# Optimization experiments

Hardware: AMD Instinct MI355X
Metric: run time of the kernel (lower is better)

The kernel has to match this reference:

```python
import jax, jax.numpy as jnp
import numpy as np

BS, T, N, E = 4, 6, 400, 3000
D = 100        # object_dim == state_dim == out_fts (forced by code)
NS = 30        # num states
NOBJ = 300     # object vocab
NET = 10       # n edge types
NSTEPS = 3     # GatedGraphConv n_steps


def setup_inputs() -> dict:
    key = jax.random.key(0)
    ks = jax.random.split(key, 16)
    def nrm(k, shape, s=0.05):
        return jax.random.normal(k, shape, jnp.float32) * s
    return dict(
        class_names=jax.random.randint(ks[0], (BS, T, N), 0, NOBJ),
        states=jax.random.uniform(ks[1], (BS, T, N, NS), jnp.float32),
        edges=jax.random.randint(ks[2], (BS, T, E, 2), 0, N),
        edge_types=jax.random.randint(ks[3], (BS, T, E), 0, NET),
        visibility=jax.random.uniform(ks[4], (BS, T, N), jnp.float32),
        mask_edges=jnp.ones((BS, T, E), jnp.float32),
        obj_emb=nrm(ks[5], (NOBJ, D)),
        state_W=nrm(ks[6], (D, NS)), state_b=jnp.zeros((D,), jnp.float32),
        c1_W=nrm(ks[7], (D, 2 * D)), c1_b=jnp.zeros((D,), jnp.float32),
        c2_W=nrm(ks[8], (D, D)), c2_b=jnp.zeros((D,), jnp.float32),
        edge_embed=nrm(ks[9], (NET, D * D)),
        g_wih=nrm(ks[10], (3 * D, D)), g_whh=nrm(ks[11], (3 * D, D)),
        g_bih=jnp.zeros((3 * D,), jnp.float32), g_bhh=jnp.zeros((3 * D,), jnp.float32),
        o_wih=nrm(ks[12], (3 * D, D)), o_whh=nrm(ks[13], (3 * D, D)),
    )


def _gru(x, h, wih, whh, bih=None, bhh=None):
    # torch.nn.GRUCell semantics
    gi = x @ wih.T
    gh = h @ whh.T
    if bih is not None:
        gi = gi + bih
        gh = gh + bhh
    ir, iz, inn = jnp.split(gi, 3, axis=-1)
    hr, hz, hn = jnp.split(gh, 3, axis=-1)
    r = jax.nn.sigmoid(ir + hr)
    z = jax.nn.sigmoid(iz + hz)
    n = jnp.tanh(inn + r * hn)
    return (1.0 - z) * n + z * h


def reference(class_names, states, edges, edge_types, visibility, mask_edges,
              obj_emb, state_W, state_b, c1_W, c1_b, c2_W, c2_b,
              edge_embed, g_wih, g_whh, g_bih, g_bhh, o_wih, o_whh):
    bs, t_len, n = class_names.shape
    # initial node representation (ClassNameStateRepresentation)
    emb = obj_emb[class_names]                       # [bs,T,N,D]
    st = states @ state_W.T + state_b                # [bs,T,N,D]
    x = jnp.concatenate([emb, st], -1)
    x = jax.nn.relu(x @ c1_W.T + c1_b) @ c2_W.T + c2_b  # [bs,T,N,D]

    off = (jnp.arange(bs) * n)[:, None]              # flatten batch into node axis
    h = jnp.zeros((bs * n, D), x.dtype)              # outer temporal GRU state
    reprs = []
    for t in range(t_len):
        h = _gru(x[:, t].reshape(bs * n, D), h, o_wih, o_whh)  # bias=False
        feat_flat = h                                 # [bs*N, D]
        src = (edges[:, t, :, 0] + off).reshape(-1)   # [bs*E]
        dst = (edges[:, t, :, 1] + off).reshape(-1)
        # per-edge DxD matrices, masked (as in original)
        W = edge_embed[edge_types[:, t].reshape(-1)].reshape(-1, D, D)
        W = W * mask_edges[:, t].reshape(-1)[:, None, None]
        # NOTE: original never updates feat_flat inside the n_steps loop,
        # so every step reads the same source features; we replicate that.
        feat_out = feat_flat
        for _ in range(NSTEPS):
            msg = jnp.einsum('eij,ej->ei', W, feat_flat[src])           # per-edge matvec
            a = jax.ops.segment_sum(msg, dst, num_segments=bs * n)     # scatter-add
            feat_out = _gru(a, feat_flat, g_wih, g_whh, g_bih, g_bhh)
        reprs.append(feat_out.reshape(bs, n, D) * visibility[:, t, :, None])
    node_reprs = jnp.stack(reprs, 1)                  # [bs,T,N,D]
    num_nodes = visibility.sum(-1) + 1e-9             # [bs,T]
    global_repr = (node_reprs * visibility[..., None]).sum(2) / num_nodes[..., None]
    return node_reprs, global_repr
```

## Files before the change

### kernel.cpp

```cpp
#include <hip/hip_runtime.h>

#define BSZ   4
#define TT    6
#define NNODE 400
#define EED   3000
#define DDIM  100
#define NSDIM 30
#define NETYP 10
#define BN    (BSZ*NNODE)
#define NROW  (BSZ*TT*NNODE)
#define NEDGE (BSZ*TT*EED)
#define KPAD  1024

#define OFF_PRE1 0
#define OFF_QT   30000
#define OFF_BQ   33000
#define OFF_BF   33104
#define OFF_WIT  33408
#define OFF_BI   63408
#define OFF_BH   63744
#define OFF_WFH  64080
#define OFF_WFL  85584
#define OFF_WOH  107088
#define OFF_WOL  128592
#define OFF_BWPK 150096
#define OFF_WHPK 322128
#define OFF_HALL 343632
#define OFF_START 1303632
#define OFF_SE   1313236
#define OFF_INV  1457248
#define OFF_GI   1457280
#define OFF_UB   4682880

typedef __attribute__((ext_vector_type(8))) short bf16x8;
typedef __attribute__((ext_vector_type(4))) float f32x4;

__device__ __forceinline__ float sigf(float v) { return 1.0f / (1.0f + expf(-v)); }

__device__ __forceinline__ short bfc(float f) {
    union { float f; unsigned u; } v; v.f = f;
    unsigned r = v.u + 0x7fffu + ((v.u >> 16) & 1u);
    return (short)(r >> 16);
}

__device__ __forceinline__ float bf2f(short h) {
    union { unsigned u; float f; } x; x.u = ((unsigned)(unsigned short)h) << 16;
    return x.f;
}

__device__ __forceinline__ unsigned cvtpk(float lo, float hi) {
    unsigned r;
    asm("v_cvt_pk_bf16_f32 %0, %1, %2" : "=v"(r) : "v"(lo), "v"(hi));
    return r;
}

__global__ __launch_bounds__(256) void k_front(
    const float* __restrict__ obj_emb, const float* __restrict__ c1_W,
    const float* __restrict__ c1_b, const float* __restrict__ state_W,
    const float* __restrict__ state_b, const float* __restrict__ c2_W,
    const float* __restrict__ c2_b, const float* __restrict__ o_wih,
    const float* __restrict__ o_whh, const float* __restrict__ g_wih,
    const float* __restrict__ g_whh,
    const float* __restrict__ g_bih, const float* __restrict__ g_bhh,
    const float* __restrict__ vis, const int* __restrict__ edges,
    const int* __restrict__ etype, const float* __restrict__ emask,
    float* __restrict__ pre1, float* __restrict__ QT, float* __restrict__ bQ,
    float* __restrict__ bfold, float* __restrict__ WiT,
    float* __restrict__ bI, float* __restrict__ bH,
    ushort* __restrict__ WFH, ushort* __restrict__ WFL,
    ushort* __restrict__ WOH, ushort* __restrict__ WOL,
    ushort* __restrict__ WHpku,
    float* __restrict__ inv_nv, float* __restrict__ gout,
    int* __restrict__ start, int2* __restrict__ sortedE2) {
    int tid = threadIdx.x;
    if (blockIdx.x < 24) {
        __shared__ int hcnt[400];
        __shared__ int hstart[400];
        int c = blockIdx.x;
        int t = c >> 2, b = c & 3;
        int febase = (b * TT + t) * EED;
        for (int i = tid; i < 400; i += 256) hcnt[i] = 0;
        __syncthreads();
        for (int i = tid; i < EED; i += 256)
            atomicAdd(&hcnt[edges[(febase + i) * 2 + 1]], 1);
        __syncthreads();
        if (tid < 64) {
            int lane = tid, carry = 0;
            for (int ch = 0; ch < 7; ++ch) {
                int idx = ch * 64 + lane;
                int orig = (idx < 400) ? hcnt[idx] : 0;
                int v = orig;
                #pragma unroll
                for (int off = 1; off < 64; off <<= 1) {
                    int u = __shfl_up(v, off, 64);
                    if (lane >= off) v += u;
                }
                if (idx < 400) hstart[idx] = carry + (v - orig);
                carry += __shfl(v, 63, 64);
            }
        }
        __syncthreads();
        for (int i = tid; i < 400; i += 256) {
            start[c * 400 + i] = c * EED + hstart[i];
            hcnt[i] = hstart[i];
        }
        if (c == 23 && tid == 0) start[NROW] = NEDGE;
        __syncthreads();
        for (int i = tid; i < EED; i += 256) {
            int fe = febase + i;
            int2 ed = *(const int2*)(edges + fe * 2);
            int pos = atomicAdd(&hcnt[ed.y], 1);
            int g = etype[fe];
            float m = emask[fe];
            sortedE2[c * EED + pos] = make_int2(ed.x | (g << 16), __float_as_int(m));
        }
        return;
    }
    int i = (blockIdx.x - 24) * 256 + tid;
    if (i < 30000) {
        int cls = i / DDIM, d1 = i % DDIM;
        float acc = 0.f;
        for (int k = 0; k < DDIM; ++k)
            acc += obj_emb[cls * DDIM + k] * c1_W[d1 * 2 * DDIM + k];
        pre1[i] = acc;
    } else if (i < 33000) {
        int j = i - 30000, s = j / DDIM, d1 = j % DDIM;
        float acc = 0.f;
        for (int d = 0; d < DDIM; ++d)
            acc += c1_W[d1 * 2 * DDIM + DDIM + d] * state_W[d * NSDIM + s];
        QT[j] = acc;
    } else if (i < 33100) {
        int d1 = i - 33000;
        float acc = c1_b[d1];
        for (int d = 0; d < DDIM; ++d)
            acc += state_b[d] * c1_W[d1 * 2 * DDIM + DDIM + d];
        bQ[d1] = acc;
    } else if (i < 33400) {
        int o = i - 33100;
        float acc = 0.f;
        for (int d = 0; d < DDIM; ++d)
            acc += o_wih[o * DDIM + d] * c2_b[d];
        bfold[o] = acc;
    } else if (i < 76408) {
        int e = i - 33400;
        int j = e & 7, frag = e >> 3;
        int l = frag & 63, ct = (frag >> 6) % 21, kt = frag / (21 * 64);
        int col = ct * 16 + (l & 15);
        int gate = col / 112, dd = col % 112;
        int k = kt * 32 + ((l >> 4) << 3) + j;
        float v = 0.f;
        if (k < DDIM && dd < DDIM) {
            int o = gate * DDIM + dd;
            for (int d = 0; d < DDIM; ++d)
                v += o_wih[o * DDIM + d] * c2_W[d * DDIM + k];
        }
        short hi = bfc(v);
        WFH[frag * 8 + j] = (ushort)hi;
        WFL[frag * 8 + j] = (ushort)bfc(v - bf2f(hi));
    } else if (i < 119416) {
        int e = i - 76408;
        int j = e & 7, frag = e >> 3;
        int l = frag & 63, ct = (frag >> 6) % 21, kt = frag / (21 * 64);
        int col = ct * 16 + (l & 15);
        int gate = col / 112, dd = col % 112;
        int k = kt * 32 + ((l >> 4) << 3) + j;
        float v = 0.f;
        if (k < DDIM && dd < DDIM)
            v = o_whh[(gate * DDIM + dd) * DDIM + k];
        short hi = bfc(v);
        WOH[frag * 8 + j] = (ushort)hi;
        WOL[frag * 8 + j] = (ushort)bfc(v - bf2f(hi));
    } else if (i < 149416) {
        int j = i - 119416, k = j / 300, o = j % 300;
        WiT[j] = g_wih[o * DDIM + k];
    } else if (i < 149752) {
        int col = i - 149416, gate = col / 112, o = col % 112;
        bI[col] = (o < DDIM) ? g_bih[gate * DDIM + o] : 0.f;
    } else if (i < 150088) {
        int col = i - 149752, gate = col / 112, o = col % 112;
        bH[col] = (o < DDIM) ? g_bhh[gate * DDIM + o] : 0.f;
    } else if (i >= 150144 && i < 151680) {
        int g = (i - 150144) >> 6;
        int lane = i & 63;
        float s = 0.f;
        for (int n = lane; n < NNODE; n += 64)
            s += vis[g * NNODE + n];
        #pragma unroll
        for (int off = 32; off > 0; off >>= 1)
            s += __shfl_down(s, off, 64);
        if (lane == 0) inv_nv[g] = 1.f / (s + 1e-9f);
    } else if (i >= 151680 && i < 154080) {
        gout[i - 151680] = 0.f;
    } else if (i >= 154080 && i < 197088) {
        int e = i - 154080;
        int j = e & 7, frag = e >> 3;
        int l = frag & 63, ct = (frag >> 6) % 21, kt2 = frag / (21 * 64);
        int col = ct * 16 + (l & 15);
        int gate = col / 112, o = col % 112;
        int k = kt2 * 32 + ((l >> 4) << 3) + j;
        float v = (k < DDIM && o < DDIM)
                  ? g_whh[(gate * DDIM + o) * DDIM + k] : 0.f;
        WHpku[frag * 8 + j] = (ushort)bfc(v);
    }
}

__global__ __launch_bounds__(448) void k_mid(
    const float* __restrict__ edge_embed, const float* __restrict__ WiT,
    const int* __restrict__ cls, const float* __restrict__ states,
    const float* __restrict__ pre1, const float* __restrict__ QT,
    const float* __restrict__ bQ, const float* __restrict__ bfold,
    const bf16x8* __restrict__ WFH, const bf16x8* __restrict__ WFL,
    float* __restrict__ GI, ushort* __restrict__ BWpku) {
    __shared__ float st_lds[16 * NSDIM];
    __shared__ float hid_lds[16 * 112];
    __shared__ int cls_lds[16];
    int tid = threadIdx.x;
    if (blockIdx.x >= 600) {
        int e = (blockIdx.x - 600) * 448 + tid;
        int j = e & 7, frag = e >> 3;
        int ll = frag & 63, ct = (frag >> 6) % 21, kt = frag / (21 * 64);
        int col = ct * 16 + (ll & 15);
        int gate = col / 112, o = col % 112;
        int kk = kt * 32 + ((ll >> 4) << 3) + j;
        float v = 0.f;
        if (kk < 1000 && o < DDIM) {
            int g = kk / DDIM, k = kk % DDIM;
            const float* es = edge_embed + g * DDIM * DDIM + k;
            const float* wt = WiT + gate * DDIM + o;
            for (int j2 = 0; j2 < DDIM; ++j2)
                v += es[j2 * DDIM] * wt[j2 * 300];
        }
        BWpku[frag * 8 + j] = (ushort)bfc(v);
        return;
    }
    int r0 = blockIdx.x * 16;
    for (int idx = tid; idx < 16 * NSDIM; idx += 448) st_lds[idx] = states[r0 * NSDIM + idx];
    if (tid < 16) cls_lds[tid] = cls[r0 + tid];
    __syncthreads();
    #pragma unroll
    for (int u = 0; u < 4; ++u) {
        int it = tid + u * 448;
        if (it < 1600) {
            int n = it / 100, d = it % 100;
            float acc = bQ[d] + pre1[cls_lds[n] * DDIM + d];
            for (int s = 0; s < NSDIM; ++s)
                acc += QT[s * DDIM + d] * st_lds[n * NSDIM + s];
            hid_lds[n * 112 + d] = fmaxf(acc, 0.f);
        }
    }
    __syncthreads();
    int w = tid >> 6, l = tid & 63, rit = l & 15, kgrp = l >> 4;
    f32x4 acc3[3];
    acc3[0] = acc3[1] = acc3[2] = (f32x4){0.f, 0.f, 0.f, 0.f};
    for (int kt = 0; kt < 4; ++kt) {
        bf16x8 Ahi, Alo;
        #pragma unroll
        for (int j = 0; j < 8; ++j) {
            int k = kt * 32 + kgrp * 8 + j;
            float v = (k < DDIM) ? hid_lds[rit * 112 + k] : 0.f;
            short hi = bfc(v);
            Ahi[j] = hi;
            Alo[j] = bfc(v - bf2f(hi));
        }
        #pragma unroll
        for (int p = 0; p < 3; ++p) {
            int ct = w + p * 7;
            bf16x8 Bhi = WFH[(kt * 21 + ct) * 64 + l];
            bf16x8 Blo = WFL[(kt * 21 + ct) * 64 + l];
            acc3[p] = __builtin_amdgcn_mfma_f32_16x16x32_bf16(Ahi, Bhi, acc3[p], 0, 0, 0);
            acc3[p] = __builtin_amdgcn_mfma_f32_16x16x32_bf16(Alo, Bhi, acc3[p], 0, 0, 0);
            acc3[p] = __builtin_amdgcn_mfma_f32_16x16x32_bf16(Ahi, Blo, acc3[p], 0, 0, 0);
        }
    }
    int dd = w * 16 + rit;
    if (dd < DDIM) {
        int b = r0 / (TT * NNODE), t = (r0 / NNODE) % TT, nn0 = r0 % NNODE;
        int trow0 = t * BN + b * NNODE + nn0;
        #pragma unroll
        for (int p = 0; p < 3; ++p) {
            float bias = bfold[p * DDIM + dd];
            #pragma unroll
            for (int j = 0; j < 4; ++j) {
                int row = kgrp * 4 + j;
                GI[(trow0 + row) * 336 + p * 112 + dd] = acc3[p][j] + bias;
            }
        }
    }
}

__global__ __launch_bounds__(448) void k_mid2(const float* __restrict__ GI,
    const bf16x8* __restrict__ WOH, const bf16x8* __restrict__ WOL,
    float* __restrict__ Hall) {
    __shared__ float h_lds[16 * 112];
    int tid = threadIdx.x;
    int bn0 = blockIdx.x * 16;
    for (int idx = tid; idx < 16 * 112; idx += 448) h_lds[idx] = 0.f;
    __syncthreads();
    int w = tid >> 6, l = tid & 63, rit = l & 15, kgrp = l >> 4;
    int dd = w * 16 + rit;
    for (int t = 0; t < TT; ++t) {
        float gir[4], giz[4], gin[4], hold[4];
        if (dd < DDIM) {
            #pragma unroll
            for (int j = 0; j < 4; ++j) {
                int node = kgrp * 4 + j;
                int trow = t * BN + bn0 + node;
                gir[j] = GI[trow * 336 + dd];
                giz[j] = GI[trow * 336 + 112 + dd];
                gin[j] = GI[trow * 336 + 224 + dd];
                hold[j] = h_lds[node * 112 + dd];
            }
        }
        f32x4 a0 = (f32x4){0.f, 0.f, 0.f, 0.f};
        f32x4 a1 = (f32x4){0.f, 0.f, 0.f, 0.f};
        f32x4 a2 = (f32x4){0.f, 0.f, 0.f, 0.f};
        if (t > 0) {
            for (int kt = 0; kt < 4; ++kt) {
                bf16x8 Ahi, Alo;
                #pragma unroll
                for (int j = 0; j < 8; ++j) {
                    int k = kt * 32 + kgrp * 8 + j;
                    float v = (k < DDIM) ? h_lds[rit * 112 + k] : 0.f;
                    short hi = bfc(v);
                    Ahi[j] = hi;
                    Alo[j] = bfc(v - bf2f(hi));
                }
                {
                    bf16x8 Bhi = WOH[(kt * 21 + w) * 64 + l];
                    bf16x8 Blo = WOL[(kt * 21 + w) * 64 + l];
                    a0 = __builtin_amdgcn_mfma_f32_16x16x32_bf16(Ahi, Bhi, a0, 0, 0, 0);
                    a0 = __builtin_amdgcn_mfma_f32_16x16x32_bf16(Alo, Bhi, a0, 0, 0, 0);
                    a0 = __builtin_amdgcn_mfma_f32_16x16x32_bf16(Ahi, Blo, a0, 0, 0, 0);
                }
                {
                    bf16x8 Bhi = WOH[(kt * 21 + w + 7) * 64 + l];
                    bf16x8 Blo = WOL[(kt * 21 + w + 7) * 64 + l];
                    a1 = __builtin_amdgcn_mfma_f32_16x16x32_bf16(Ahi, Bhi, a1, 0, 0, 0);
                    a1 = __builtin_amdgcn_mfma_f32_16x16x32_bf16(Alo, Bhi, a1, 0, 0, 0);
                    a1 = __builtin_amdgcn_mfma_f32_16x16x32_bf16(Ahi, Blo, a1, 0, 0, 0);
                }
                {
                    bf16x8 Bhi = WOH[(kt * 21 + w + 14) * 64 + l];
                    bf16x8 Blo = WOL[(kt * 21 + w + 14) * 64 + l];
                    a2 = __builtin_amdgcn_mfma_f32_16x16x32_bf16(Ahi, Bhi, a2, 0, 0, 0);
                    a2 = __builtin_amdgcn_mfma_f32_16x16x32_bf16(Alo, Bhi, a2, 0, 0, 0);
                    a2 = __builtin_amdgcn_mfma_f32_16x16x32_bf16(Ahi, Blo, a2, 0, 0, 0);
                }
            }
        }
        __syncthreads();
        if (dd < DDIM) {
            #pragma unroll
            for (int j = 0; j < 4; ++j) {
                int node = kgrp * 4 + j;
                int trow = t * BN + bn0 + node;
                float r = sigf(gir[j] + a0[j]);
                float z = sigf(giz[j] + a1[j]);
                float nn = tanhf(gin[j] + r * a2[j]);
                float hnew = (1.f - z) * nn + z * hold[j];
                h_lds[node * 112 + dd] = hnew;
                Hall[trow * DDIM + dd] = hnew;
            }
        }
        __syncthreads();
    }
}

__global__ __launch_bounds__(256) void k_gather(
    const int* __restrict__ start, const int2* __restrict__ sortedE2,
    const float* __restrict__ Hall, unsigned* __restrict__ Ub2) {
    int gid = blockIdx.x * 256 + threadIdx.x;
    int trd = gid >> 6, l = gid & 63;
    int s0 = start[trd], s1 = start[trd + 1];
    int rowbase = (trd / NNODE) * NNODE;
    float acc[16];
    #pragma unroll
    for (int j = 0; j < 16; ++j) acc[j] = 0.f;
    for (int e0 = s0; e0 < s1; e0 += 4) {
        float2 hA[4], hB[4];
        float me[4];
        int ge[4];
        #pragma unroll
        for (int e = 0; e < 4; ++e) {
            int idx = e0 + e;
            int2 rec = (idx < s1) ? sortedE2[idx] : make_int2(0, 0);
            int src = rec.x & 0xffff;
            int g = rec.x >> 16;
            ge[e] = g;
            me[e] = __int_as_float(rec.y);
            const float* hs = Hall + (size_t)(rowbase + src) * DDIM;
            int k0 = g * 100;
            int J0 = k0 >> 7, J1 = (k0 + 99) >> 7;
            int sA = 128 * J0 + 2 * l, sB = 128 * J1 + 2 * l;
            bool aA = (sA >= k0) && (sA < k0 + 100);
            bool aB = (J1 != J0) && (sB >= k0) && (sB < k0 + 100);
            hA[e] = aA ? *(const float2*)(hs + (sA - k0)) : make_float2(0.f, 0.f);
            hB[e] = aB ? *(const float2*)(hs + (sB - k0)) : make_float2(0.f, 0.f);
        }
        #pragma unroll
        for (int e = 0; e < 4; ++e) {
            float m = me[e];
            float ax = m * hA[e].x, ay = m * hA[e].y;
            float bx = m * hB[e].x, by = m * hB[e].y;
            switch (ge[e]) {
                case 0: acc[0] += ax; acc[1] += ay; break;
                case 1: acc[0] += ax; acc[1] += ay; acc[2] += bx; acc[3] += by; break;
                case 2: acc[2] += ax; acc[3] += ay; acc[4] += bx; acc[5] += by; break;
                case 3: acc[4] += ax; acc[5] += ay; acc[6] += bx; acc[7] += by; break;
                case 4: acc[6] += ax; acc[7] += ay; break;
                case 5: acc[6] += ax; acc[7] += ay; acc[8] += bx; acc[9] += by; break;
                case 6: acc[8] += ax; acc[9] += ay; acc[10] += bx; acc[11] += by; break;
                case 7: acc[10] += ax; acc[11] += ay; acc[12] += bx; acc[13] += by; break;
                case 8: acc[12] += ax; acc[13] += ay; acc[14] += bx; acc[15] += by; break;
                case 9: acc[14] += ax; acc[15] += ay; break;
            }
        }
    }
    unsigned* urow = Ub2 + (size_t)trd * 512;
    #pragma unroll
    for (int j = 0; j < 8; ++j)
        urow[64 * j + l] = cvtpk(acc[2 * j], acc[2 * j + 1]);
}

__global__ __launch_bounds__(448) void k_fused32(const ushort* __restrict__ Ub,
    const bf16x8* __restrict__ BWpk, const bf16x8* __restrict__ WHpk,
    const float* __restrict__ bI, const float* __restrict__ bH,
    const float* __restrict__ Hall, const float* __restrict__ visv,
    const float* __restrict__ inv_nv, float* __restrict__ out,
    float* __restrict__ gout) {
    __shared__ unsigned lds[16384];
    int tid = threadIdx.x;
    int w = tid >> 6, l = tid & 63;
    int rit = l & 15, kgrp = l >> 4;
    int rbase = blockIdx.x * 32;

    for (int i = tid; i < 4096; i += 448) {
        int row = i >> 7, g16 = i & 127;
        int4 wv = *(const int4*)(Ub + (size_t)(rbase + row) * KPAD + g16 * 8);
        int wd = row * 512 + ((g16 * 4) ^ ((row & 7) << 2));
        *(int4*)&lds[wd] = wv;
    }
    __syncthreads();

    f32x4 acc[2][3];
    #pragma unroll
    for (int mt = 0; mt < 2; ++mt)
        #pragma unroll
        for (int q = 0; q < 3; ++q) acc[mt][q] = (f32x4){0.f, 0.f, 0.f, 0.f};

    for (int kt = 0; kt < 32; ++kt) {
        bf16x8 fb0 = BWpk[(kt * 21 + w) * 64 + l];
        bf16x8 fb1 = BWpk[(kt * 21 + w + 7) * 64 + l];
        bf16x8 fb2 = BWpk[(kt * 21 + w + 14) * 64 + l];
        #pragma unroll
        for (int mt = 0; mt < 2; ++mt) {
            int row = mt * 16 + rit;
            int wd = row * 512 + (((kt * 16 + kgrp * 4)) ^ ((row & 7) << 2));
            bf16x8 fa = *(bf16x8*)&lds[wd];
            acc[mt][0] = __builtin_amdgcn_mfma_f32_16x16x32_bf16(fa, fb0, acc[mt][0], 0, 0, 0);
            acc[mt][1] = __builtin_amdgcn_mfma_f32_16x16x32_bf16(fa, fb1, acc[mt][1], 0, 0, 0);
            acc[mt][2] = __builtin_amdgcn_mfma_f32_16x16x32_bf16(fa, fb2, acc[mt][2], 0, 0, 0);
        }
    }
    __syncthreads();

    for (int i = tid; i < 512; i += 448) {
        int row = i >> 4, g16 = i & 15;
        int k0 = g16 * 8;
        const float* hs = Hall + (size_t)(rbase + row) * DDIM;
        float v[8];
        #pragma unroll
        for (int jj = 0; jj < 8; ++jj)
            v[jj] = (k0 + jj < DDIM) ? hs[k0 + jj] : 0.f;
        int4 wv;
        wv.x = (int)cvtpk(v[0], v[1]);
        wv.y = (int)cvtpk(v[2], v[3]);
        wv.z = (int)cvtpk(v[4], v[5]);
        wv.w = (int)cvtpk(v[6], v[7]);
        int wd = row * 64 + ((g16 * 4) ^ ((row & 7) << 2));
        *(int4*)&lds[wd] = wv;
    }
    __syncthreads();

    f32x4 hacc[2];
    hacc[0] = (f32x4){0.f, 0.f, 0.f, 0.f};
    hacc[1] = (f32x4){0.f, 0.f, 0.f, 0.f};
    for (int kt2 = 0; kt2 < 4; ++kt2) {
        bf16x8 fb0 = WHpk[(kt2 * 21 + w) * 64 + l];
        bf16x8 fb1 = WHpk[(kt2 * 21 + w + 7) * 64 + l];
        bf16x8 fb2 = WHpk[(kt2 * 21 + w + 14) * 64 + l];
        #pragma unroll
        for (int mt = 0; mt < 2; ++mt) {
            int row = mt * 16 + rit;
            int wd = row * 64 + (((kt2 * 16 + kgrp * 4)) ^ ((row & 7) << 2));
            bf16x8 fh = *(bf16x8*)&lds[wd];
            acc[mt][0] = __builtin_amdgcn_mfma_f32_16x16x32_bf16(fh, fb0, acc[mt][0], 0, 0, 0);
            acc[mt][1] = __builtin_amdgcn_mfma_f32_16x16x32_bf16(fh, fb1, acc[mt][1], 0, 0, 0);
            hacc[mt]  = __builtin_amdgcn_mfma_f32_16x16x32_bf16(fh, fb2, hacc[mt], 0, 0, 0);
        }
    }

    int col = w * 16 + rit;
    if (col < DDIM) {
        float bIr = bI[col], bIz = bI[112 + col], bIn = bI[224 + col];
        float bHr = bH[col], bHz = bH[112 + col], bHn = bH[224 + col];
        int t = rbase / BN;
        #pragma unroll
        for (int mt = 0; mt < 2; ++mt) {
            int r2 = (rbase + mt * 16) % BN;
            int b = r2 / NNODE, n0 = r2 % NNODE;
            int bt = b * TT + t;
            int trow0 = rbase + mt * 16 + kgrp * 4;
            int brow0 = bt * NNODE + n0 + kgrp * 4;
            float gs = 0.f;
            #pragma unroll
            for (int j = 0; j < 4; ++j) {
                float r = sigf(acc[mt][0][j] + bIr + bHr);
                float z = sigf(acc[mt][1][j] + bIz + bHz);
                float ghn = hacc[mt][j] + bHn;
                float nn = tanhf(acc[mt][2][j] + bIn + r * ghn);
                float hold = Hall[(trow0 + j) * DDIM + col];
                float feat = (1.f - z) * nn + z * hold;
                int brow = brow0 + j;
                float v = visv[brow];
                float outv = feat * v;
                out[brow * DDIM + col] = outv;
                gs += outv * v;
            }
            gs += __shfl_xor(gs, 16, 64);
            gs += __shfl_xor(gs, 32, 64);
            if (kgrp == 0)
                atomicAdd(&gout[bt * DDIM + col], gs * inv_nv[bt]);
        }
    }
}

extern "C" void kernel_launch(void* const* d_in, const int* in_sizes, int n_in,
                              void* d_out, int out_size, void* d_ws, size_t ws_size,
                              hipStream_t stream) {
    const int*   class_names = (const int*)d_in[0];
    const float* states      = (const float*)d_in[1];
    const int*   edges       = (const int*)d_in[2];
    const int*   edge_types  = (const int*)d_in[3];
    const float* visibility  = (const float*)d_in[4];
    const float* mask_edges  = (const float*)d_in[5];
    const float* obj_emb     = (const float*)d_in[6];
    const float* state_W     = (const float*)d_in[7];
    const float* state_b     = (const float*)d_in[8];
    const float* c1_W        = (const float*)d_in[9];
    const float* c1_b        = (const float*)d_in[10];
    const float* c2_W        = (const float*)d_in[11];
    const float* c2_b        = (const float*)d_in[12];
    const float* edge_embed  = (const float*)d_in[13];
    const float* g_wih       = (const float*)d_in[14];
    const float* g_whh       = (const float*)d_in[15];
    const float* g_bih       = (const float*)d_in[16];
    const float* g_bhh       = (const float*)d_in[17];
    const float* o_wih       = (const float*)d_in[18];
    const float* o_whh       = (const float*)d_in[19];

    float* out = (float*)d_out;
    float* gout = out + (size_t)NROW * DDIM;
    float* ws  = (float*)d_ws;
    float*  pre1  = ws + OFF_PRE1;
    float*  QT    = ws + OFF_QT;
    float*  bQ    = ws + OFF_BQ;
    float*  bfold = ws + OFF_BF;
    float*  WiT   = ws + OFF_WIT;
    float*  bI    = ws + OFF_BI;
    float*  bH    = ws + OFF_BH;
    ushort* WFH   = (ushort*)(ws + OFF_WFH);
    ushort* WFL   = (ushort*)(ws + OFF_WFL);
    ushort* WOH   = (ushort*)(ws + OFF_WOH);
    ushort* WOL   = (ushort*)(ws + OFF_WOL);
    ushort* BWpku = (ushort*)(ws + OFF_BWPK);
    ushort* WHpku = (ushort*)(ws + OFF_WHPK);
    float*  Hall  = ws + OFF_HALL;
    int*    start = (int*)(ws + OFF_START);
    int2*   sortedE2 = (int2*)(ws + OFF_SE);
    float*  inv_nv= ws + OFF_INV;
    float*  GI    = ws + OFF_GI;
    ushort* Ub    = (ushort*)(ws + OFF_UB);

    k_front<<<794, 256, 0, stream>>>(obj_emb, c1_W, c1_b, state_W, state_b,
                                     c2_W, c2_b, o_wih, o_whh, g_wih, g_whh,
                                     g_bih, g_bhh, visibility, edges, edge_types,
                                     mask_edges, pre1, QT, bQ, bfold, WiT,
                                     bI, bH, WFH, WFL, WOH, WOL, WHpku,
                                     inv_nv, gout, start, sortedE2);
    k_mid<<<1368, 448, 0, stream>>>(edge_embed, WiT, class_names, states,
                                    pre1, QT, bQ, bfold,
                                    (const bf16x8*)WFH, (const bf16x8*)WFL,
                                    GI, BWpku);
    k_mid2<<<100, 448, 0, stream>>>(GI, (const bf16x8*)WOH, (const bf16x8*)WOL,
                                    Hall);
    k_gather<<<NROW / 4, 256, 0, stream>>>(start, sortedE2, Hall, (unsigned*)Ub);
    k_fused32<<<NROW / 32, 448, 0, stream>>>(Ub, (const bf16x8*)BWpku,
                                             (const bf16x8*)WHpku, bI, bH, Hall,
                                             visibility, inv_nv, out, gout);
}
```

Measured before the change: 105.1 us.

## Compute folded edge-embed×W_ih weights with split-bf16 MFMA instead of scalar loops

The folded per-edge-type input weight (edge_embed composed with the GRU input weight) was built with 768 blocks, where each thread ran a 100-term scalar dot product. It is now built with 10 blocks, one per edge type, using MFMA 16x16x32 with a hi/lo bf16 split to stay close to fp32 accuracy. To support this, the front kernel pre-packs g_wih into hi/lo MFMA fragments instead of a transposed fp32 copy. The aim is to shrink the weight-folding cost inside k_mid. The trade-off is that only 10 blocks now do that work, which could serialize on a few CUs.

```diff
diff --git a/kernel.cpp b/kernel.cpp
--- a/kernel.cpp
+++ b/kernel.cpp
@@ -16,21 +16,22 @@
 #define OFF_QT   30000
 #define OFF_BQ   33000
 #define OFF_BF   33104
-#define OFF_WIT  33408
-#define OFF_BI   63408
-#define OFF_BH   63744
-#define OFF_WFH  64080
-#define OFF_WFL  85584
-#define OFF_WOH  107088
-#define OFF_WOL  128592
-#define OFF_BWPK 150096
-#define OFF_WHPK 322128
-#define OFF_HALL 343632
-#define OFF_START 1303632
-#define OFF_SE   1313236
-#define OFF_INV  1457248
-#define OFF_GI   1457280
-#define OFF_UB   4682880
+#define OFF_WIH  33408
+#define OFF_WIL  54912
+#define OFF_BI   76416
+#define OFF_BH   76752
+#define OFF_WFH  77088
+#define OFF_WFL  98592
+#define OFF_WOH  120096
+#define OFF_WOL  141600
+#define OFF_BWPK 163104
+#define OFF_WHPK 335136
+#define OFF_HALL 356640
+#define OFF_START 1316640
+#define OFF_SE   1326244
+#define OFF_INV  1470272
+#define OFF_GI   1470304
+#define OFF_UB   4695904
 
 typedef __attribute__((ext_vector_type(8))) short bf16x8;
 typedef __attribute__((ext_vector_type(4))) float f32x4;
@@ -65,7 +66,8 @@
     const float* __restrict__ vis, const int* __restrict__ edges,
     const int* __restrict__ etype, const float* __restrict__ emask,
     float* __restrict__ pre1, float* __restrict__ QT, float* __restrict__ bQ,
-    float* __restrict__ bfold, float* __restrict__ WiT,
+    float* __restrict__ bfold,
+    ushort* __restrict__ WIH, ushort* __restrict__ WIL,
     float* __restrict__ bI, float* __restrict__ bH,
     ushort* __restrict__ WFH, ushort* __restrict__ WFL,
     ushort* __restrict__ WOH, ushort* __restrict__ WOL,
@@ -170,17 +172,27 @@
         short hi = bfc(v);
         WOH[frag * 8 + j] = (ushort)hi;
         WOL[frag * 8 + j] = (ushort)bfc(v - bf2f(hi));
-    } else if (i < 149416) {
-        int j = i - 119416, k = j / 300, o = j % 300;
-        WiT[j] = g_wih[o * DDIM + k];
-    } else if (i < 149752) {
-        int col = i - 149416, gate = col / 112, o = col % 112;
+    } else if (i < 162424) {
+        int e = i - 119416;
+        int j = e & 7, frag = e >> 3;
+        int l = frag & 63, ct = (frag >> 6) % 21, kt = frag / (21 * 64);
+        int col = ct * 16 + (l & 15);
+        int gate = col / 112, dd = col % 112;
+        int jrow = kt * 32 + ((l >> 4) << 3) + j;
+        float v = 0.f;
+        if (jrow < DDIM && dd < DDIM)
+            v = g_wih[(gate * DDIM + dd) * DDIM + jrow];
+        short hi = bfc(v);
+        WIH[frag * 8 + j] = (ushort)hi;
+        WIL[frag * 8 + j] = (ushort)bfc(v - bf2f(hi));
+    } else if (i < 162760) {
+        int col = i - 162424, gate = col / 112, o = col % 112;
         bI[col] = (o < DDIM) ? g_bih[gate * DDIM + o] : 0.f;
-    } else if (i < 150088) {
-        int col = i - 149752, gate = col / 112, o = col % 112;
+    } else if (i < 163096) {
+        int col = i - 162760, gate = col / 112, o = col % 112;
         bH[col] = (o < DDIM) ? g_bhh[gate * DDIM + o] : 0.f;
-    } else if (i >= 150144 && i < 151680) {
-        int g = (i - 150144) >> 6;
+    } else if (i >= 163136 && i < 164672) {
+        int g = (i - 163136) >> 6;
         int lane = i & 63;
         float s = 0.f;
         for (int n = lane; n < NNODE; n += 64)
@@ -189,10 +201,10 @@
         for (int off = 32; off > 0; off >>= 1)
             s += __shfl_down(s, off, 64);
         if (lane == 0) inv_nv[g] = 1.f / (s + 1e-9f);
-    } else if (i >= 151680 && i < 154080) {
-        gout[i - 151680] = 0.f;
-    } else if (i >= 154080 && i < 197088) {
-        int e = i - 154080;
+    } else if (i >= 164672 && i < 167072) {
+        gout[i - 164672] = 0.f;
+    } else if (i >= 167072 && i < 210080) {
+        int e = i - 167072;
         int j = e & 7, frag = e >> 3;
         int l = frag & 63, ct = (frag >> 6) % 21, kt2 = frag / (21 * 64);
         int col = ct * 16 + (l & 15);
@@ -205,32 +217,72 @@
 }
 
 __global__ __launch_bounds__(448) void k_mid(
-    const float* __restrict__ edge_embed, const float* __restrict__ WiT,
+    const float* __restrict__ edge_embed,
     const int* __restrict__ cls, const float* __restrict__ states,
     const float* __restrict__ pre1, const float* __restrict__ QT,
     const float* __restrict__ bQ, const float* __restrict__ bfold,
     const bf16x8* __restrict__ WFH, const bf16x8* __restrict__ WFL,
+    const bf16x8* __restrict__ WIH, const bf16x8* __restrict__ WIL,
     float* __restrict__ GI, ushort* __restrict__ BWpku) {
     __shared__ float st_lds[16 * NSDIM];
     __shared__ float hid_lds[16 * 112];
     __shared__ int cls_lds[16];
     int tid = threadIdx.x;
+    int w = tid >> 6, l = tid & 63, rit = l & 15, kgrp = l >> 4;
     if (blockIdx.x >= 600) {
-        int e = (blockIdx.x - 600) * 448 + tid;
-        int j = e & 7, frag = e >> 3;
-        int ll = frag & 63, ct = (frag >> 6) % 21, kt = frag / (21 * 64);
-        int col = ct * 16 + (ll & 15);
-        int gate = col / 112, o = col % 112;
-        int kk = kt * 32 + ((ll >> 4) << 3) + j;
-        float v = 0.f;
-        if (kk < 1000 && o < DDIM) {
-            int g = kk / DDIM, k = kk % DDIM;
-            const float* es = edge_embed + g * DDIM * DDIM + k;
-            const float* wt = WiT + gate * DDIM + o;
-            for (int j2 = 0; j2 < DDIM; ++j2)
-                v += es[j2 * DDIM] * wt[j2 * 300];
-        }
-        BWpku[frag * 8 + j] = (ushort)bfc(v);
+        int g = blockIdx.x - 600;
+        const float* Eg = edge_embed + g * DDIM * DDIM;
+        int rt = w;
+        for (int p = 0; p < 3; ++p) {
+            f32x4 a7[7];
+            #pragma unroll
+            for (int c = 0; c < 7; ++c) a7[c] = (f32x4){0.f, 0.f, 0.f, 0.f};
+            for (int kt = 0; kt < 4; ++kt) {
+                bf16x8 Ahi, Alo;
+                #pragma unroll
+                for (int jj = 0; jj < 8; ++jj) {
+                    int j = kt * 32 + (kgrp << 3) + jj;
+                    int kr = rt * 16 + rit;
+                    float v = (j < DDIM && kr < DDIM) ? Eg[j * DDIM + kr] : 0.f;
+                    short hi = bfc(v);
+                    Ahi[jj] = hi;
+                    Alo[jj] = bfc(v - bf2f(hi));
+                }
+                #pragma unroll
+                for (int c = 0; c < 7; ++c) {
+                    int ct = p * 7 + c;
+                    bf16x8 Bhi = WIH[(kt * 21 + ct) * 64 + l];
+                    bf16x8 Blo = WIL[(kt * 21 + ct) * 64 + l];
+                    a7[c] = __builtin_amdgcn_mfma_f32_16x16x32_bf16(Ahi, Bhi, a7[c], 0, 0, 0);
+                    a7[c] = __builtin_amdgcn_mfma_f32_16x16x32_bf16(Alo, Bhi, a7[c], 0, 0, 0);
+                    a7[c] = __builtin_amdgcn_mfma_f32_16x16x32_bf16(Ahi, Blo, a7[c], 0, 0, 0);
+                }
+            }
+            #pragma unroll
+            for (int c = 0; c < 7; ++c) {
+                int ct = p * 7 + c;
+                #pragma unroll
+                for (int q = 0; q < 4; ++q) {
+                    int kloc = rt * 16 + kgrp * 4 + q;
+                    if (kloc < DDIM) {
+                        int kk = g * DDIM + kloc;
+                        int kto = kk >> 5, r5 = kk & 31;
+                        int lt = ((r5 >> 3) << 4) + rit;
+                        BWpku[((kto * 21 + ct) * 64 + lt) * 8 + (r5 & 7)] =
+                            (ushort)bfc(a7[c][q]);
+                    }
+                }
+            }
+        }
+        if (g == 9) {
+            for (int idx = tid; idx < 24 * 336; idx += 448) {
+                int kk = 1000 + idx / 336;
+                int col = idx % 336;
+                int r5 = kk & 31;
+                int lt = ((r5 >> 3) << 4) + (col & 15);
+                BWpku[((31 * 21 + (col >> 4)) * 64 + lt) * 8 + (r5 & 7)] = 0;
+            }
+        }
         return;
     }
     int r0 = blockIdx.x * 16;
@@ -249,7 +301,6 @@
         }
     }
     __syncthreads();
-    int w = tid >> 6, l = tid & 63, rit = l & 15, kgrp = l >> 4;
     f32x4 acc3[3];
     acc3[0] = acc3[1] = acc3[2] = (f32x4){0.f, 0.f, 0.f, 0.f};
     for (int kt = 0; kt < 4; ++kt) {
@@ -566,7 +617,8 @@
     float*  QT    = ws + OFF_QT;
     float*  bQ    = ws + OFF_BQ;
     float*  bfold = ws + OFF_BF;
-    float*  WiT   = ws + OFF_WIT;
+    ushort* WIH   = (ushort*)(ws + OFF_WIH);
+    ushort* WIL   = (ushort*)(ws + OFF_WIL);
     float*  bI    = ws + OFF_BI;
     float*  bH    = ws + OFF_BH;
     ushort* WFH   = (ushort*)(ws + OFF_WFH);
@@ -582,16 +634,17 @@
     float*  GI    = ws + OFF_GI;
     ushort* Ub    = (ushort*)(ws + OFF_UB);
 
-    k_front<<<794, 256, 0, stream>>>(obj_emb, c1_W, c1_b, state_W, state_b,
+    k_front<<<845, 256, 0, stream>>>(obj_emb, c1_W, c1_b, state_W, state_b,
                                      c2_W, c2_b, o_wih, o_whh, g_wih, g_whh,
                                      g_bih, g_bhh, visibility, edges, edge_types,
-                                     mask_edges, pre1, QT, bQ, bfold, WiT,
+                                     mask_edges, pre1, QT, bQ, bfold, WIH, WIL,
                                      bI, bH, WFH, WFL, WOH, WOL, WHpku,
                                      inv_nv, gout, start, sortedE2);
-    k_mid<<<1368, 448, 0, stream>>>(edge_embed, WiT, class_names, states,
-                                    pre1, QT, bQ, bfold,
-                                    (const bf16x8*)WFH, (const bf16x8*)WFL,
-                                    GI, BWpku);
+    k_mid<<<610, 448, 0, stream>>>(edge_embed, class_names, states,
+                                   pre1, QT, bQ, bfold,
+                                   (const bf16x8*)WFH, (const bf16x8*)WFL,
+                                   (const bf16x8*)WIH, (const bf16x8*)WIL,
+                                   GI, BWpku);
     k_mid2<<<100, 448, 0, stream>>>(GI, (const bf16x8*)WOH, (const bf16x8*)WOL,
                                     Hall);
     k_gather<<<NROW / 4, 256, 0, stream>>>(start, sortedE2, Hall, (unsigned*)Ub);
```

Result: slower. 123.8 us (+17.8%).
